# Performance work log

Hardware: AMD Instinct MI355X
Metric: run time of the kernel (lower is better)

Reference implementation:

```python
import jax, jax.numpy as jnp
import numpy as np

RESO = 32          # triplane/voxel resolution
VIT = 16           # ViT patch grid resolution
PAD = 0.1
C_TRI = 64         # triplane channels per plane
C_IMG = 1280       # image feature channels
C_IN = 128         # inner (attention) channels
C_OUT = 64
NH = 8
HD = C_IN // NH
IMG_SIZE = 224.0


def pos_enc(d_model, length):
    pos = jnp.arange(length, dtype=jnp.float32)[:, None]
    div = jnp.exp(jnp.arange(0, d_model, 2, dtype=jnp.float32) * (-np.log(10000.0) / d_model))
    pe = jnp.zeros((length, d_model), jnp.float32)
    pe = pe.at[:, 0::2].set(jnp.sin(pos * div))
    pe = pe.at[:, 1::2].set(jnp.cos(pos * div))
    return pe


def bilinear_sample(feats, gx, gy):
    # feats: [B, J, H, W, C]; gx, gy: [B, J, N] in [-1, 1]; align_corners=True
    B, J, Hh, Ww, _ = feats.shape
    ux = (gx + 1.0) * 0.5 * (Ww - 1)
    uy = (gy + 1.0) * 0.5 * (Hh - 1)
    x0 = jnp.floor(ux).astype(jnp.int32)
    y0 = jnp.floor(uy).astype(jnp.int32)
    wx = (ux - x0)[..., None]
    wy = (uy - y0)[..., None]
    x1 = jnp.clip(x0 + 1, 0, Ww - 1)
    y1 = jnp.clip(y0 + 1, 0, Hh - 1)
    x0 = jnp.clip(x0, 0, Ww - 1)
    y0 = jnp.clip(y0, 0, Hh - 1)
    bi = jnp.arange(B)[:, None, None]
    ji = jnp.arange(J)[None, :, None]
    f00 = feats[bi, ji, y0, x0]
    f01 = feats[bi, ji, y0, x1]
    f10 = feats[bi, ji, y1, x0]
    f11 = feats[bi, ji, y1, x1]
    return (f00 * (1 - wx) * (1 - wy) + f01 * wx * (1 - wy)
            + f10 * (1 - wx) * wy + f11 * wx * wy)


def forward(triplane_feat, image_feat, proj_mat, k_w, k_b, q_w, q_b, v_w, v_b,
            in_w, in_b, out_w, out_b, proj_w, proj_b):
    B, n_img = image_feat.shape[0], image_feat.shape[1]
    N = RESO ** 3
    img = image_feat[:, :, 1:, :]                        # drop CLS -> [B,J,256,C_IMG]
    image_pe = pos_enc(C_IN, VIT * VIT)[None, None]      # [1,1,256,C_IN]
    k_feat = img @ k_w.T + k_b + image_pe
    v_feat = img @ v_w.T + v_b + image_pe
    k_map = k_feat.reshape(B, n_img, VIT, VIT, C_IN)     # [B,J,H,W,C]
    v_map = v_feat.reshape(B, n_img, VIT, VIT, C_IN)

    # voxel coords -> project into each camera
    idx = jnp.arange(RESO)
    X, Y, Z = jnp.meshgrid(idx, idx, idx, indexing='ij')
    vox = jnp.stack([X, Y, Z], -1).reshape(N, 3).astype(jnp.float32)
    vox = (vox / (RESO - 1) - 0.5) * 2.0 * (1.0 + PAD + 1e-5)
    homo = jnp.concatenate([vox, jnp.ones((N, 1), jnp.float32)], -1)  # [N,4]
    pc = jnp.einsum('nk,bjik->bjni', homo, proj_mat)                   # [B,J,N,4]
    px = pc[..., 0] / pc[..., 2]
    py = pc[..., 1] / pc[..., 2]
    gx = jnp.clip((px / (IMG_SIZE - 1) - 0.5) * 2.0, -1.0, 1.0)
    gy = jnp.clip((py / (IMG_SIZE - 1) - 0.5) * 2.0, -1.0, 1.0)
    # The torch code does a 3D grid_sample whose depth coordinate lands exactly
    # on each image index (align_corners=True), so it reduces to per-image
    # bilinear sampling on the 16x16 token maps.
    k_s = bilinear_sample(k_map, gx, gy)   # [B,J,N,C_IN]
    v_s = bilinear_sample(v_map, gx, gy)

    # triplane features expanded to the voxel grid (voxel order n = x*R^2+y*R+z)
    xz, xy, yz = jnp.split(triplane_feat, 3, axis=2)     # each [B,C,R,R]
    xz_t = jnp.transpose(xz, (0, 3, 2, 1))               # [B,x,z,C]
    xy_t = jnp.transpose(xy, (0, 3, 2, 1))               # [B,x,y,C]
    yz_t = jnp.transpose(yz, (0, 3, 2, 1))               # [B,y,z,C]
    shp = (B, RESO, RESO, RESO, C_TRI)
    xz_v = jnp.broadcast_to(xz_t[:, :, None, :, :], shp)
    xy_v = jnp.broadcast_to(xy_t[:, :, :, None, :], shp)
    yz_v = jnp.broadcast_to(yz_t[:, None, :, :, :], shp)
    tri = jnp.concatenate([xz_v, xy_v, yz_v], -1).reshape(B, N, 3 * C_TRI)
    q = tri @ q_w.T + q_b + pos_enc(C_IN, N)[None]       # [B,N,C_IN]

    # per-voxel cross attention (q_len=1, kv_len=n_img); torch MHA semantics
    Wq, Wk, Wv = in_w[:C_IN], in_w[C_IN:2 * C_IN], in_w[2 * C_IN:]
    bq, bk, bv = in_b[:C_IN], in_b[C_IN:2 * C_IN], in_b[2 * C_IN:]
    qh = (q @ Wq.T + bq).reshape(B, N, NH, HD)
    k_t = jnp.transpose(k_s, (0, 2, 1, 3))               # [B,N,J,C]
    v_t = jnp.transpose(v_s, (0, 2, 1, 3))
    kh = (k_t @ Wk.T + bk).reshape(B, N, n_img, NH, HD)
    vh = (v_t @ Wv.T + bv).reshape(B, N, n_img, NH, HD)
    logits = jnp.einsum('bnhd,bnjhd->bnhj', qh, kh) / np.sqrt(HD).astype(np.float32)
    attn = jax.nn.softmax(logits, axis=-1)
    o = jnp.einsum('bnhj,bnjhd->bnhd', attn, vh).reshape(B, N, C_IN)
    o = o @ out_w.T + out_b

    # mean-pool volume back to three planes
    vol = o.reshape(B, RESO, RESO, RESO, C_IN)             # [b,x,y,z,c]
    xz_o = jnp.transpose(vol.mean(axis=2), (0, 2, 1, 3))   # [b,z,x,c]
    xy_o = jnp.transpose(vol.mean(axis=3), (0, 2, 1, 3))   # [b,y,x,c]
    yz_o = jnp.transpose(vol.mean(axis=1), (0, 2, 1, 3))   # [b,z,y,c]
    planes = jnp.concatenate([xz_o, xy_o, yz_o], axis=1)   # [B,3R,R,C_IN]
    out = planes @ proj_w.T + proj_b
    return jnp.transpose(out, (0, 3, 1, 2))                # [B,C_OUT,3R,R]


def setup_inputs() -> dict:
    key = jax.random.key(0)
    ks = jax.random.split(key, 10)
    B, J = 2, 5
    s = 0.02
    base = jnp.array([[200., 0., 112., 0.],
                      [0., 200., 112., 0.],
                      [0., 0., 1., 3.5],
                      [0., 0., 0., 1.]], jnp.float32)
    return {
        'triplane_feat': jax.random.normal(ks[0], (B, C_TRI, 3 * RESO, RESO), jnp.float32),
        'image_feat': jax.random.normal(ks[1], (B, J, VIT * VIT + 1, C_IMG), jnp.float32),
        'proj_mat': base[None, None] + 0.01 * jax.random.normal(ks[2], (B, J, 4, 4), jnp.float32),
        'valid_frames': jnp.ones((B, J), jnp.int32),
        'k_w': s * jax.random.normal(ks[3], (C_IN, C_IMG), jnp.float32), 'k_b': jnp.zeros((C_IN,), jnp.float32),
        'q_w': s * jax.random.normal(ks[4], (C_IN, 3 * C_TRI), jnp.float32), 'q_b': jnp.zeros((C_IN,), jnp.float32),
        'v_w': s * jax.random.normal(ks[5], (C_IN, C_IMG), jnp.float32), 'v_b': jnp.zeros((C_IN,), jnp.float32),
        'in_w': s * jax.random.normal(ks[6], (3 * C_IN, C_IN), jnp.float32), 'in_b': jnp.zeros((3 * C_IN,), jnp.float32),
        'out_w': s * jax.random.normal(ks[7], (C_IN, C_IN), jnp.float32), 'out_b': jnp.zeros((C_IN,), jnp.float32),
        'proj_w': s * jax.random.normal(ks[8], (C_OUT, C_IN), jnp.float32), 'proj_b': jnp.zeros((C_OUT,), jnp.float32),
    }


def reference(triplane_feat, image_feat, proj_mat, valid_frames, k_w, k_b, q_w, q_b,
              v_w, v_b, in_w, in_b, out_w, out_b, proj_w, proj_b):
    # valid_frames matches the torch forward signature but is unused in its body
    return forward(triplane_feat, image_feat, proj_mat, k_w, k_b, q_w, q_b,
                   v_w, v_b, in_w, in_b, out_w, out_b, proj_w, proj_b)
```

## Files before the change

### kernel.cpp

```cpp
#include <hip/hip_runtime.h>
#include <hip/hip_bf16.h>
#include <cstddef>

#define NVOX 32768
#define J5 5
typedef __hip_bfloat16 bf16;
typedef __attribute__((ext_vector_type(8))) short bf16x8v;
typedef __attribute__((ext_vector_type(4))) float f32x4;

static __device__ __forceinline__ float pe_val(int pos, int c) {
  float dv = expf((float)(c & ~1) * (-0.0719557841560639f));
  float arg = (float)pos * dv;
  return (c & 1) ? cosf(arg) : sinf(arg);
}
static __device__ __forceinline__ short f2b(float f) {
  __hip_bfloat16 h = __float2bfloat16(f);
  return *reinterpret_cast<short*>(&h);
}
static __device__ __forceinline__ float b2f(short s) {
  __hip_bfloat16 h = *reinterpret_cast<__hip_bfloat16*>(&s);
  return __bfloat162float(h);
}
static __device__ __forceinline__ float2 cmul(float2 a, float2 b) {
  return make_float2(a.x * b.x - a.y * b.y, a.x * b.y + a.y * b.x);
}

#define NB_TABS   24
#define NB_WQPE   64
#define NB_WQC    96
#define NB_WO     32
#define NB_QCB    1
#define NB_CVT    1600
#define NB_TRI    1536
#define NB_FOLDW  1280
#define NB_PEB    512
#define B_TABS   0
#define B_WQPE   (B_TABS + NB_TABS)
#define B_WQC    (B_WQPE + NB_WQPE)
#define B_WO     (B_WQC + NB_WQC)
#define B_QCB    (B_WO + NB_WO)
#define B_CVT    (B_QCB + NB_QCB)
#define B_TRI    (B_CVT + NB_CVT)
#define B_FOLDW  (B_TRI + NB_TRI)
#define B_PEB    (B_FOLDW + NB_FOLDW)
#define NB_TOTAL (B_PEB + NB_PEB)

__global__ __launch_bounds__(256) void k_prep(
    const float* __restrict__ img, const float* __restrict__ tp,
    const float* __restrict__ k_w, const float* __restrict__ k_b,
    const float* __restrict__ q_w, const float* __restrict__ q_b,
    const float* __restrict__ v_w, const float* __restrict__ v_b,
    const float* __restrict__ in_w, const float* __restrict__ in_b,
    const float* __restrict__ out_w, const float* __restrict__ out_b,
    const float* __restrict__ proj_w, const float* __restrict__ proj_b,
    float2* __restrict__ tabs, short* __restrict__ Wqb_s, float* __restrict__ Wo,
    float* __restrict__ qcb, float* __restrict__ obb, short* __restrict__ imgb,
    short* __restrict__ tri_tb, short* __restrict__ Wkvb_s, float* __restrict__ peb) {
  __shared__ float s_pe[128];
  const int bx = blockIdx.x, t = threadIdx.x;

  if (bx < B_WQPE) {
    int idx = bx * 256 + t;
    if (idx < 6144) {
      int tb = idx >> 11, rem = idx & 2047;
      int pos = rem >> 6, i = rem & 63;
      float dv = expf((float)(2 * i) * (-0.0719557841560639f));
      float mult = (tb == 0) ? 1024.0f : (tb == 1) ? 32.0f : 1.0f;
      float ang = (float)pos * mult * dv;
      tabs[idx] = make_float2(cosf(ang), sinf(ang));
    }
  } else if (bx < B_WQC) {
    int e = (bx - B_WQPE) * 256 + t;
    int c = e >> 7, j = e & 127;
    Wqb_s[(size_t)c * 320 + 192 + j] = f2b(in_w[(size_t)c * 128 + j]);
  } else if (bx < B_WO) {
    int e = (bx - B_WQC) * 256 + t;
    int c = e / 192, k = e % 192;
    const float* ir = in_w + (size_t)c * 128;
    float acc = 0.f;
    for (int j = 0; j < 128; j++) acc = fmaf(ir[j], q_w[(size_t)j * 192 + k], acc);
    Wqb_s[(size_t)c * 320 + k] = f2b(acc);
  } else if (bx < B_QCB) {
    int e = (bx - B_WO) * 256 + t;
    int o = e >> 7, c = e & 127;
    const float* pr = proj_w + (size_t)o * 128;
    float acc = 0.f;
    for (int j = 0; j < 128; j++) acc = fmaf(pr[j], out_w[(size_t)j * 128 + c], acc);
    Wo[e] = acc;
  } else if (bx < B_CVT) {
    if (t < 128) {
      float acc = in_b[t];
      const float* ir = in_w + (size_t)t * 128;
      for (int j = 0; j < 128; j++) acc = fmaf(ir[j], q_b[j], acc);
      qcb[t] = acc;
    }
    if (t < 64) {
      float acc = proj_b[t];
      const float* pr = proj_w + (size_t)t * 128;
      for (int j = 0; j < 128; j++) acc = fmaf(pr[j], out_b[j], acc);
      obb[t] = acc;
    }
  } else if (bx < B_TRI) {
    int e8 = (bx - B_CVT) * 256 + t;
    int row = e8 / 160, k8 = e8 % 160;
    int bj = row >> 8, p = row & 255;
    const float* src = img + ((size_t)(bj * 257 + 1 + p)) * 1280 + k8 * 8;
    float4 a = *(const float4*)src;
    float4 b = *(const float4*)(src + 4);
    bf16x8v v;
    v[0] = f2b(a.x); v[1] = f2b(a.y); v[2] = f2b(a.z); v[3] = f2b(a.w);
    v[4] = f2b(b.x); v[5] = f2b(b.y); v[6] = f2b(b.z); v[7] = f2b(b.w);
    *reinterpret_cast<bf16x8v*>(imgb + (size_t)row * 1280 + k8 * 8) = v;
  } else if (bx < B_FOLDW) {
    int idx = (bx - B_TRI) * 256 + t;
    int cc   = idx & 63;
    int rem  = idx >> 6;
    int cell = rem & 1023;
    int segb = rem >> 10;
    int seg = segb % 3, b = segb / 3;
    int i = cell >> 5, j = cell & 31;
    tri_tb[idx] = f2b(tp[(((size_t)(b * 64 + cc)) * 96 + seg * 32 + i) * 32 + j]);
  } else if (bx < B_PEB) {
    int u = (bx - B_FOLDW) * 256 + t;
    int c = u / 1280, k = u % 1280;
    const float* w = (c < 128) ? k_w : v_w;
    const float* ir = in_w + (size_t)(128 + c) * 128;
    float acc = 0.f;
    for (int j = 0; j < 128; j++) acc = fmaf(ir[j], w[(size_t)j * 1280 + k], acc);
    Wkvb_s[(size_t)c * 1280 + k] = f2b(acc);
  } else {
    int e = bx - B_PEB;
    int which = e >> 8, p = e & 255;
    if (t < 128) {
      const float* bias = which ? v_b : k_b;
      s_pe[t] = bias[t] + pe_val(p, t);
    }
    __syncthreads();
    if (t < 128) {
      int c = t;
      const float* wr = in_w + (size_t)(128 + which * 128 + c) * 128;
      float acc = in_b[128 + which * 128 + c];
      for (int j = 0; j < 128; j++) acc = fmaf(s_pe[j], wr[j], acc);
      peb[((size_t)(which * 256 + p)) * 128 + c] = acc;
    }
  }
}

__global__ __launch_bounds__(256) void k_gemm_kv(
    const short* __restrict__ imgb, const short* __restrict__ Wkvb_s,
    const float* __restrict__ peb, short* __restrict__ k2b, short* __restrict__ v2b) {
  __shared__ __align__(16) short A_lds[64 * 64];
  __shared__ __align__(16) short B_lds[64 * 64];
  const int m0 = blockIdx.x * 64;
  const int nb0 = blockIdx.y * 64;
  const int t = threadIdx.x;
  const int lane = t & 63, w = t >> 6;
  f32x4 acc[4];
#pragma unroll
  for (int f = 0; f < 4; f++) acc[f] = (f32x4){0.f, 0.f, 0.f, 0.f};

  for (int ct = 0; ct < 20; ct++) {
    __syncthreads();
#pragma unroll
    for (int it = 0; it < 2; it++) {
      int u = it * 256 + t;
      int r = u >> 3, g = u & 7;
      {
        const int4 src = *reinterpret_cast<const int4*>(imgb + (size_t)(m0 + r) * 1280 + ct * 64 + g * 8);
        *reinterpret_cast<int4*>(&A_lds[(r * 8 + (g ^ (r & 7))) * 8]) = src;
      }
      {
        const int4 src = *reinterpret_cast<const int4*>(Wkvb_s + (size_t)(nb0 + r) * 1280 + ct * 64 + g * 8);
        *reinterpret_cast<int4*>(&B_lds[(r * 8 + (g ^ (r & 7))) * 8]) = src;
      }
    }
    __syncthreads();
#pragma unroll
    for (int ks = 0; ks < 2; ks++) {
      int arow = w * 16 + (lane & 15);
      int akb = ks * 4 + (lane >> 4);
      bf16x8v a = *reinterpret_cast<const bf16x8v*>(&A_lds[(arow * 8 + (akb ^ (arow & 7))) * 8]);
#pragma unroll
      for (int f = 0; f < 4; f++) {
        int bcol = f * 16 + (lane & 15);
        bf16x8v bb = *reinterpret_cast<const bf16x8v*>(&B_lds[(bcol * 8 + (akb ^ (bcol & 7))) * 8]);
        acc[f] = __builtin_amdgcn_mfma_f32_16x16x32_bf16(a, bb, acc[f], 0, 0, 0);
      }
    }
  }
#pragma unroll
  for (int f = 0; f < 4; f++) {
#pragma unroll
    for (int reg = 0; reg < 4; reg++) {
      int grow = m0 + w * 16 + (lane >> 4) * 4 + reg;
      int gcol = nb0 + f * 16 + (lane & 15);
      int p = grow & 255;
      int which = gcol >> 7, c = gcol & 127;
      float val = acc[f][reg] + peb[((size_t)(which * 256 + p)) * 128 + c];
      short* dst = which ? v2b : k2b;
      dst[(size_t)grow * 128 + c] = f2b(val);
    }
  }
}

__global__ __launch_bounds__(256) void k_main(
    const short* __restrict__ tri_tb, const short* __restrict__ Wqb_s,
    const float* __restrict__ qcb, const float2* __restrict__ tabs,
    const short* __restrict__ k2b, const short* __restrict__ v2b,
    const float* __restrict__ proj, bf16* __restrict__ obuf) {
  __shared__ __align__(16) short A_lds[32 * 64];
  __shared__ __align__(16) short B_lds[128 * 64];
  __shared__ __align__(16) short qh_lds[32 * 128];
  __shared__ __align__(16) ushort sIr[160][4];
  __shared__ __align__(16) float sW4[160][4];
  __shared__ __align__(16) float lg[160 * 8];
  const int b = blockIdx.y;
  const int n0 = blockIdx.x * 32;
  const int t = threadIdx.x;
  const int lane = t & 63, w = t >> 6;
  const int xq = n0 >> 10, yq = (n0 >> 5) & 31;
  const float2* tabX = tabs;
  const float2* tabY = tabs + 2048;
  const float2* tabZ = tabs + 4096;

  if (t < 160) {
    int r = t / J5, j = t % J5;
    int n = n0 + r;
    int x = n >> 10, y = (n >> 5) & 31, z = n & 31;
    const float SC = (float)(1.0 + 0.1 + 1e-05);
    float fx = ((float)x / 31.0f - 0.5f) * 2.0f * SC;
    float fy = ((float)y / 31.0f - 0.5f) * 2.0f * SC;
    float fz = ((float)z / 31.0f - 0.5f) * 2.0f * SC;
    const float* P = proj + (size_t)(b * J5 + j) * 16;
    float pc0 = fmaf(fx, P[0], fmaf(fy, P[1], fmaf(fz, P[2],  P[3])));
    float pc1 = fmaf(fx, P[4], fmaf(fy, P[5], fmaf(fz, P[6],  P[7])));
    float pc2 = fmaf(fx, P[8], fmaf(fy, P[9], fmaf(fz, P[10], P[11])));
    float px = pc0 / pc2, py = pc1 / pc2;
    float gx = fminf(fmaxf((px / 223.0f - 0.5f) * 2.0f, -1.0f), 1.0f);
    float gy = fminf(fmaxf((py / 223.0f - 0.5f) * 2.0f, -1.0f), 1.0f);
    float ux = (gx + 1.0f) * 0.5f * 15.0f;
    float uy = (gy + 1.0f) * 0.5f * 15.0f;
    float fx0 = floorf(ux), fy0 = floorf(uy);
    int x0 = (int)fx0, y0 = (int)fy0;
    float wx = ux - fx0, wy = uy - fy0;
    int x1 = min(x0 + 1, 15), y1 = min(y0 + 1, 15);
    x0 = min(max(x0, 0), 15); y0 = min(max(y0, 0), 15);
    int rowb = (b * J5 + j) * 256;
    sIr[t][0] = (ushort)(rowb + y0 * 16 + x0);
    sIr[t][1] = (ushort)(rowb + y0 * 16 + x1);
    sIr[t][2] = (ushort)(rowb + y1 * 16 + x0);
    sIr[t][3] = (ushort)(rowb + y1 * 16 + x1);
    sW4[t][0] = (1.f - wx) * (1.f - wy);
    sW4[t][1] = wx * (1.f - wy);
    sW4[t][2] = (1.f - wx) * wy;
    sW4[t][3] = wx * wy;
  }

  f32x4 acc[2][2];
#pragma unroll
  for (int m = 0; m < 2; m++)
#pragma unroll
    for (int f = 0; f < 2; f++) acc[m][f] = (f32x4){0.f, 0.f, 0.f, 0.f};

  for (int ct = 0; ct < 5; ct++) {
    __syncthreads();
    {
      int r = t >> 3, g = t & 7;
      if (ct < 3) {
        int n = n0 + r;
        int x = n >> 10, y = (n >> 5) & 31, z = n & 31;
        int cell = (ct == 0) ? (z * 32 + x) : (ct == 1) ? (y * 32 + x) : (z * 32 + y);
        const int4 src = *reinterpret_cast<const int4*>(
            tri_tb + ((size_t)(b * 3 + ct) * 1024 + cell) * 64 + g * 8);
        *reinterpret_cast<int4*>(&A_lds[(r * 8 + (g ^ (r & 7))) * 8]) = src;
      } else {
        int i0 = (ct - 3) * 32 + g * 4;
        bf16x8v v;
#pragma unroll
        for (int q = 0; q < 4; q++) {
          int i = i0 + q;
          float2 exy = cmul(tabX[xq * 64 + i], tabY[yq * 64 + i]);
          float2 e = cmul(exy, tabZ[r * 64 + i]);
          v[q * 2]     = f2b(e.y);
          v[q * 2 + 1] = f2b(e.x);
        }
        *reinterpret_cast<bf16x8v*>(&A_lds[(r * 8 + (g ^ (r & 7))) * 8]) = v;
      }
    }
    {
#pragma unroll
      for (int it = 0; it < 4; it++) {
        int u = it * 256 + t;
        int col = u >> 3, g = u & 7;
        const int4 src = *reinterpret_cast<const int4*>(
            Wqb_s + (size_t)col * 320 + ct * 64 + g * 8);
        *reinterpret_cast<int4*>(&B_lds[(col * 8 + (g ^ (col & 7))) * 8]) = src;
      }
    }
    __syncthreads();
#pragma unroll
    for (int ks = 0; ks < 2; ks++) {
      int kb = ks * 4 + (lane >> 4);
      bf16x8v a[2], bb[2];
#pragma unroll
      for (int m = 0; m < 2; m++) {
        int row = m * 16 + (lane & 15);
        a[m] = *reinterpret_cast<const bf16x8v*>(&A_lds[(row * 8 + (kb ^ (row & 7))) * 8]);
      }
#pragma unroll
      for (int f = 0; f < 2; f++) {
        int col = w * 32 + f * 16 + (lane & 15);
        bb[f] = *reinterpret_cast<const bf16x8v*>(&B_lds[(col * 8 + (kb ^ (col & 7))) * 8]);
      }
#pragma unroll
      for (int m = 0; m < 2; m++)
#pragma unroll
        for (int f = 0; f < 2; f++)
          acc[m][f] = __builtin_amdgcn_mfma_f32_16x16x32_bf16(a[m], bb[f], acc[m][f], 0, 0, 0);
    }
  }
#pragma unroll
  for (int m = 0; m < 2; m++)
#pragma unroll
    for (int f = 0; f < 2; f++)
#pragma unroll
      for (int reg = 0; reg < 4; reg++) {
        int row = m * 16 + (lane >> 4) * 4 + reg;
        int col = w * 32 + f * 16 + (lane & 15);
        qh_lds[row * 128 + col] = f2b(acc[m][f][reg] + qcb[col]);
      }
  __syncthreads();

  {
    const int oct = t & 15, rjIdx = t >> 4;
    const int c0 = oct * 8;
#pragma unroll
    for (int it = 0; it < 10; it++) {
      int rj = rjIdx + it * 16;
      int r = rj / J5;
      ushort4 I4 = *reinterpret_cast<const ushort4*>(sIr[rj]);
      float4 W4 = *reinterpret_cast<const float4*>(sW4[rj]);
      bf16x8v t0 = *reinterpret_cast<const bf16x8v*>(k2b + (size_t)I4.x * 128 + c0);
      bf16x8v t1 = *reinterpret_cast<const bf16x8v*>(k2b + (size_t)I4.y * 128 + c0);
      bf16x8v t2 = *reinterpret_cast<const bf16x8v*>(k2b + (size_t)I4.z * 128 + c0);
      bf16x8v t3 = *reinterpret_cast<const bf16x8v*>(k2b + (size_t)I4.w * 128 + c0);
      bf16x8v q8 = *reinterpret_cast<const bf16x8v*>(&qh_lds[r * 128 + c0]);
      float pv = 0.f;
#pragma unroll
      for (int e = 0; e < 8; e++) {
        float kh = fmaf(W4.x, b2f(t0[e]), fmaf(W4.y, b2f(t1[e]),
                   fmaf(W4.z, b2f(t2[e]), W4.w * b2f(t3[e]))));
        pv = fmaf(b2f(q8[e]), kh, pv);
      }
      pv += __shfl_xor(pv, 1);
      if (!(oct & 1)) lg[rj * 8 + (oct >> 1)] = pv * 0.25f;
    }
  }
  __syncthreads();

  {
    int r = t >> 3, h = t & 7;
    float l[J5];
    float m = -1e30f;
#pragma unroll
    for (int j = 0; j < J5; j++) { l[j] = lg[(r * J5 + j) * 8 + h]; m = fmaxf(m, l[j]); }
    float sden = 0.f;
#pragma unroll
    for (int j = 0; j < J5; j++) { l[j] = expf(l[j] - m); sden += l[j]; }
    float inv = 1.0f / sden;
#pragma unroll
    for (int j = 0; j < J5; j++) lg[(r * J5 + j) * 8 + h] = l[j] * inv;
  }
  __syncthreads();

  {
    const int oct = t & 15;
    const int c0 = oct * 8;
#pragma unroll
    for (int it = 0; it < 2; it++) {
      int r = (t >> 4) + it * 16;
      float o8[8] = {0.f, 0.f, 0.f, 0.f, 0.f, 0.f, 0.f, 0.f};
#pragma unroll
      for (int j = 0; j < J5; j++) {
        int rj = r * J5 + j;
        float aw = lg[rj * 8 + (oct >> 1)];
        ushort4 I4 = *reinterpret_cast<const ushort4*>(sIr[rj]);
        float4 W4 = *reinterpret_cast<const float4*>(sW4[rj]);
        float w0 = aw * W4.x, w1 = aw * W4.y, w2 = aw * W4.z, w3 = aw * W4.w;
        bf16x8v t0 = *reinterpret_cast<const bf16x8v*>(v2b + (size_t)I4.x * 128 + c0);
        bf16x8v t1 = *reinterpret_cast<const bf16x8v*>(v2b + (size_t)I4.y * 128 + c0);
        bf16x8v t2 = *reinterpret_cast<const bf16x8v*>(v2b + (size_t)I4.z * 128 + c0);
        bf16x8v t3 = *reinterpret_cast<const bf16x8v*>(v2b + (size_t)I4.w * 128 + c0);
#pragma unroll
        for (int e = 0; e < 8; e++) {
          o8[e] = fmaf(w0, b2f(t0[e]), o8[e]);
          o8[e] = fmaf(w1, b2f(t1[e]), o8[e]);
          o8[e] = fmaf(w2, b2f(t2[e]), o8[e]);
          o8[e] = fmaf(w3, b2f(t3[e]), o8[e]);
        }
      }
      bf16x8v out;
#pragma unroll
      for (int e = 0; e < 8; e++) out[e] = f2b(o8[e]);
      *reinterpret_cast<bf16x8v*>((short*)obuf + ((size_t)b * NVOX + n0 + r) * 128 + c0) = out;
    }
  }
}

__global__ __launch_bounds__(128) void k_reduce(const bf16* __restrict__ obuf,
                                                float* __restrict__ pacc) {
  int blk = blockIdx.x;
  int b = blockIdx.y;
  int t = threadIdx.x;
  int quad = t & 31, sub = t >> 5;
  int c0 = quad * 4;
  int cell = blk * 4 + sub;
  const ushort* ob = (const ushort*)obuf + (size_t)b * NVOX * 128;
  float4 acc = {0.f, 0.f, 0.f, 0.f};
  if (cell < 1024) {
    int z = cell >> 5, x = cell & 31;
    for (int y = 0; y < 32; y++) {
      ushort4 u = *(const ushort4*)(ob + ((size_t)(x * 1024 + y * 32 + z) * 128 + c0));
      acc.x += b2f((short)u.x); acc.y += b2f((short)u.y);
      acc.z += b2f((short)u.z); acc.w += b2f((short)u.w);
    }
    *(float4*)(&pacc[((size_t)(b * 96 + z) * 32 + x) * 128 + c0]) = acc;
  } else if (cell < 2048) {
    int e = cell - 1024;
    int y = e >> 5, x = e & 31;
    for (int z = 0; z < 32; z++) {
      ushort4 u = *(const ushort4*)(ob + ((size_t)(x * 1024 + y * 32 + z) * 128 + c0));
      acc.x += b2f((short)u.x); acc.y += b2f((short)u.y);
      acc.z += b2f((short)u.z); acc.w += b2f((short)u.w);
    }
    *(float4*)(&pacc[((size_t)(b * 96 + 32 + y) * 32 + x) * 128 + c0]) = acc;
  } else {
    int e = cell - 2048;
    int z = e >> 5, y = e & 31;
    for (int x = 0; x < 32; x++) {
      ushort4 u = *(const ushort4*)(ob + ((size_t)(x * 1024 + y * 32 + z) * 128 + c0));
      acc.x += b2f((short)u.x); acc.y += b2f((short)u.y);
      acc.z += b2f((short)u.z); acc.w += b2f((short)u.w);
    }
    *(float4*)(&pacc[((size_t)(b * 96 + 64 + z) * 32 + y) * 128 + c0]) = acc;
  }
}

__global__ __launch_bounds__(128) void k_final(
    const float* __restrict__ pacc, const float* __restrict__ Wo,
    const float* __restrict__ obb, float* __restrict__ outp) {
  int bp = blockIdx.x;
  int b = bp / 96, prow = bp % 96;
  int obase = blockIdx.y * 16;
  __shared__ __align__(16) float lds[32 * 129];
  for (int idx = threadIdx.x; idx < 4096; idx += 128) {
    int col = idx >> 7, k = idx & 127;
    lds[col * 129 + k] = pacc[(size_t)bp * 32 * 128 + idx] * (1.0f / 32.0f);
  }
  __syncthreads();
  for (int e = threadIdx.x; e < 16 * 32; e += 128) {
    int o = obase + (e >> 5), col = e & 31;
    float val = obb[o];
    const float* wr = Wo + (size_t)o * 128;
    const float* lr = lds + col * 129;
    for (int k = 0; k < 128; k++) val = fmaf(wr[k], lr[k], val);
    outp[((size_t)(b * 64 + o) * 96 + prow) * 32 + col] = val;
  }
}

extern "C" void kernel_launch(void* const* d_in, const int* in_sizes, int n_in,
                              void* d_out, int out_size, void* d_ws, size_t ws_size,
                              hipStream_t stream) {
  const float* tp     = (const float*)d_in[0];
  const float* img    = (const float*)d_in[1];
  const float* proj   = (const float*)d_in[2];
  const float* k_w    = (const float*)d_in[4];
  const float* k_b    = (const float*)d_in[5];
  const float* q_w    = (const float*)d_in[6];
  const float* q_b    = (const float*)d_in[7];
  const float* v_w    = (const float*)d_in[8];
  const float* v_b    = (const float*)d_in[9];
  const float* in_w   = (const float*)d_in[10];
  const float* in_b   = (const float*)d_in[11];
  const float* out_w  = (const float*)d_in[12];
  const float* out_b  = (const float*)d_in[13];
  const float* proj_w = (const float*)d_in[14];
  const float* proj_b = (const float*)d_in[15];
  const int B = 2;

  float* ws = (float*)d_ws;
  size_t off = 0;
  short*  tri_tb = (short*)(ws + off);  off += 196608;
  short*  Wkvb_s = (short*)(ws + off);  off += 163840;
  short*  Wqb_s  = (short*)(ws + off);  off += 20480;
  float*  peb    = ws + off;            off += 65536;
  float2* tabs   = (float2*)(ws + off); off += 12288;
  float*  qcb    = ws + off;            off += 128;
  float*  Wo     = ws + off;            off += 8192;
  float*  obb    = ws + off;            off += 64;
  short*  k2b    = (short*)(ws + off);  off += 163840;
  short*  v2b    = (short*)(ws + off);  off += 163840;
  float*  pacc   = ws + off;            off += 786432;
  float*  zone   = ws + off;            off += 4194304;
  short*  imgb   = (short*)zone;
  bf16*   obuf   = (bf16*)zone;
  if (ws_size < off * sizeof(float)) return;

  k_prep<<<dim3(NB_TOTAL), dim3(256), 0, stream>>>(
      img, tp, k_w, k_b, q_w, q_b, v_w, v_b, in_w, in_b, out_w, out_b, proj_w, proj_b,
      tabs, Wqb_s, Wo, qcb, obb, imgb, tri_tb, Wkvb_s, peb);
  k_gemm_kv<<<dim3(40, 4), dim3(256), 0, stream>>>(imgb, Wkvb_s, peb, k2b, v2b);
  k_main<<<dim3(NVOX / 32, B), dim3(256), 0, stream>>>(
      tri_tb, Wqb_s, qcb, tabs, k2b, v2b, proj, obuf);
  k_reduce<<<dim3(768, B), dim3(128), 0, stream>>>(obuf, pacc);
  k_final<<<dim3(B * 96, 4), dim3(128), 0, stream>>>(pacc, Wo, obb, (float*)d_out);
}
```

Before: 117.5 us.

## Fold PE and bias into KV GEMM K-dim, retile GEMM, drop Wq LDS staging, widen reduce

```diff
diff --git a/kernel.cpp b/kernel.cpp
--- a/kernel.cpp
+++ b/kernel.cpp
@@ -4,6 +4,7 @@
 
 #define NVOX 32768
 #define J5 5
+#define KB2 1472
 typedef __hip_bfloat16 bf16;
 typedef __attribute__((ext_vector_type(8))) short bf16x8v;
 typedef __attribute__((ext_vector_type(4))) float f32x4;
@@ -33,7 +34,9 @@
 #define NB_CVT    1600
 #define NB_TRI    1536
 #define NB_FOLDW  1280
-#define NB_PEB    512
+#define NB_PETAB  128
+#define NB_WIN    128
+#define NB_CB     1
 #define B_TABS   0
 #define B_WQPE   (B_TABS + NB_TABS)
 #define B_WQC    (B_WQPE + NB_WQPE)
@@ -42,8 +45,10 @@
 #define B_CVT    (B_QCB + NB_QCB)
 #define B_TRI    (B_CVT + NB_CVT)
 #define B_FOLDW  (B_TRI + NB_TRI)
-#define B_PEB    (B_FOLDW + NB_FOLDW)
-#define NB_TOTAL (B_PEB + NB_PEB)
+#define B_PETAB  (B_FOLDW + NB_FOLDW)
+#define B_WIN    (B_PETAB + NB_PETAB)
+#define B_CB     (B_WIN + NB_WIN)
+#define NB_TOTAL (B_CB + NB_CB)
 
 __global__ __launch_bounds__(256) void k_prep(
     const float* __restrict__ img, const float* __restrict__ tp,
@@ -55,8 +60,7 @@
     const float* __restrict__ proj_w, const float* __restrict__ proj_b,
     float2* __restrict__ tabs, short* __restrict__ Wqb_s, float* __restrict__ Wo,
     float* __restrict__ qcb, float* __restrict__ obb, short* __restrict__ imgb,
-    short* __restrict__ tri_tb, short* __restrict__ Wkvb_s, float* __restrict__ peb) {
-  __shared__ float s_pe[128];
+    short* __restrict__ tri_tb, short* __restrict__ Wkvb2, short* __restrict__ pe_tab) {
   const int bx = blockIdx.x, t = threadIdx.x;
 
   if (bx < B_WQPE) {
@@ -120,85 +124,98 @@
     int seg = segb % 3, b = segb / 3;
     int i = cell >> 5, j = cell & 31;
     tri_tb[idx] = f2b(tp[(((size_t)(b * 64 + cc)) * 96 + seg * 32 + i) * 32 + j]);
-  } else if (bx < B_PEB) {
+  } else if (bx < B_PETAB) {
     int u = (bx - B_FOLDW) * 256 + t;
     int c = u / 1280, k = u % 1280;
     const float* w = (c < 128) ? k_w : v_w;
     const float* ir = in_w + (size_t)(128 + c) * 128;
     float acc = 0.f;
     for (int j = 0; j < 128; j++) acc = fmaf(ir[j], w[(size_t)j * 1280 + k], acc);
-    Wkvb_s[(size_t)c * 1280 + k] = f2b(acc);
+    Wkvb2[(size_t)c * KB2 + k] = f2b(acc);
+  } else if (bx < B_WIN) {
+    int e = (bx - B_PETAB) * 256 + t;
+    int p = e >> 7, c = e & 127;
+    pe_tab[e] = f2b(pe_val(p, c));
+  } else if (bx < B_CB) {
+    int e = (bx - B_WIN) * 256 + t;
+    int c = e >> 7, j = e & 127;
+    Wkvb2[(size_t)c * KB2 + 1280 + j] = f2b(in_w[(size_t)(128 + c) * 128 + j]);
   } else {
-    int e = bx - B_PEB;
-    int which = e >> 8, p = e & 255;
-    if (t < 128) {
-      const float* bias = which ? v_b : k_b;
-      s_pe[t] = bias[t] + pe_val(p, t);
-    }
-    __syncthreads();
-    if (t < 128) {
-      int c = t;
-      const float* wr = in_w + (size_t)(128 + which * 128 + c) * 128;
-      float acc = in_b[128 + which * 128 + c];
-      for (int j = 0; j < 128; j++) acc = fmaf(s_pe[j], wr[j], acc);
-      peb[((size_t)(which * 256 + p)) * 128 + c] = acc;
-    }
+    int c = t;
+    int which = c >> 7;
+    const float* bias = which ? v_b : k_b;
+    const float* ir = in_w + (size_t)(128 + c) * 128;
+    float acc = in_b[128 + c];
+    for (int j = 0; j < 128; j++) acc = fmaf(bias[j], ir[j], acc);
+    short* row = Wkvb2 + (size_t)c * KB2 + 1408;
+    row[0] = f2b(acc);
+    for (int k = 1; k < 64; k++) row[k] = 0;
   }
 }
 
 __global__ __launch_bounds__(256) void k_gemm_kv(
-    const short* __restrict__ imgb, const short* __restrict__ Wkvb_s,
-    const float* __restrict__ peb, short* __restrict__ k2b, short* __restrict__ v2b) {
-  __shared__ __align__(16) short A_lds[64 * 64];
+    const short* __restrict__ imgb, const short* __restrict__ Wkvb2,
+    const short* __restrict__ pe_tab, short* __restrict__ k2b, short* __restrict__ v2b) {
+  __shared__ __align__(16) short A_lds[32 * 64];
   __shared__ __align__(16) short B_lds[64 * 64];
-  const int m0 = blockIdx.x * 64;
+  const int m0 = blockIdx.x * 32;
   const int nb0 = blockIdx.y * 64;
   const int t = threadIdx.x;
   const int lane = t & 63, w = t >> 6;
-  f32x4 acc[4];
-#pragma unroll
-  for (int f = 0; f < 4; f++) acc[f] = (f32x4){0.f, 0.f, 0.f, 0.f};
-
-  for (int ct = 0; ct < 20; ct++) {
+  const int wm = w & 1, wn = w >> 1;
+  f32x4 acc[2];
+  acc[0] = (f32x4){0.f, 0.f, 0.f, 0.f};
+  acc[1] = (f32x4){0.f, 0.f, 0.f, 0.f};
+
+  for (int ct = 0; ct < 23; ct++) {
     __syncthreads();
-#pragma unroll
-    for (int it = 0; it < 2; it++) {
-      int u = it * 256 + t;
-      int r = u >> 3, g = u & 7;
-      {
-        const int4 src = *reinterpret_cast<const int4*>(imgb + (size_t)(m0 + r) * 1280 + ct * 64 + g * 8);
-        *reinterpret_cast<int4*>(&A_lds[(r * 8 + (g ^ (r & 7))) * 8]) = src;
-      }
-      {
-        const int4 src = *reinterpret_cast<const int4*>(Wkvb_s + (size_t)(nb0 + r) * 1280 + ct * 64 + g * 8);
-        *reinterpret_cast<int4*>(&B_lds[(r * 8 + (g ^ (r & 7))) * 8]) = src;
+    {
+      int r = t >> 3, g = t & 7;
+      bf16x8v v;
+      if (ct < 20) {
+        v = *reinterpret_cast<const bf16x8v*>(imgb + (size_t)(m0 + r) * 1280 + ct * 64 + g * 8);
+      } else if (ct < 22) {
+        int p = (m0 + r) & 255;
+        v = *reinterpret_cast<const bf16x8v*>(pe_tab + (size_t)p * 128 + (ct - 20) * 64 + g * 8);
+      } else {
+        v = (bf16x8v){0, 0, 0, 0, 0, 0, 0, 0};
+        if (g == 0) v[0] = (short)0x3F80;
+      }
+      *reinterpret_cast<bf16x8v*>(&A_lds[(r * 8 + (g ^ (r & 7))) * 8]) = v;
+    }
+    {
+#pragma unroll
+      for (int it = 0; it < 2; it++) {
+        int u = it * 256 + t;
+        int r2 = u >> 3, g = u & 7;
+        const int4 src = *reinterpret_cast<const int4*>(
+            Wkvb2 + (size_t)(nb0 + r2) * KB2 + ct * 64 + g * 8);
+        *reinterpret_cast<int4*>(&B_lds[(r2 * 8 + (g ^ (r2 & 7))) * 8]) = src;
       }
     }
     __syncthreads();
 #pragma unroll
     for (int ks = 0; ks < 2; ks++) {
-      int arow = w * 16 + (lane & 15);
-      int akb = ks * 4 + (lane >> 4);
-      bf16x8v a = *reinterpret_cast<const bf16x8v*>(&A_lds[(arow * 8 + (akb ^ (arow & 7))) * 8]);
-#pragma unroll
-      for (int f = 0; f < 4; f++) {
-        int bcol = f * 16 + (lane & 15);
-        bf16x8v bb = *reinterpret_cast<const bf16x8v*>(&B_lds[(bcol * 8 + (akb ^ (bcol & 7))) * 8]);
+      int kb = ks * 4 + (lane >> 4);
+      int arow = wm * 16 + (lane & 15);
+      bf16x8v a = *reinterpret_cast<const bf16x8v*>(&A_lds[(arow * 8 + (kb ^ (arow & 7))) * 8]);
+#pragma unroll
+      for (int f = 0; f < 2; f++) {
+        int bcol = wn * 32 + f * 16 + (lane & 15);
+        bf16x8v bb = *reinterpret_cast<const bf16x8v*>(&B_lds[(bcol * 8 + (kb ^ (bcol & 7))) * 8]);
         acc[f] = __builtin_amdgcn_mfma_f32_16x16x32_bf16(a, bb, acc[f], 0, 0, 0);
       }
     }
   }
 #pragma unroll
-  for (int f = 0; f < 4; f++) {
+  for (int f = 0; f < 2; f++) {
 #pragma unroll
     for (int reg = 0; reg < 4; reg++) {
-      int grow = m0 + w * 16 + (lane >> 4) * 4 + reg;
-      int gcol = nb0 + f * 16 + (lane & 15);
-      int p = grow & 255;
+      int grow = m0 + wm * 16 + (lane >> 4) * 4 + reg;
+      int gcol = nb0 + wn * 32 + f * 16 + (lane & 15);
       int which = gcol >> 7, c = gcol & 127;
-      float val = acc[f][reg] + peb[((size_t)(which * 256 + p)) * 128 + c];
       short* dst = which ? v2b : k2b;
-      dst[(size_t)grow * 128 + c] = f2b(val);
+      dst[(size_t)grow * 128 + c] = f2b(acc[f][reg]);
     }
   }
 }
@@ -209,7 +226,6 @@
     const short* __restrict__ k2b, const short* __restrict__ v2b,
     const float* __restrict__ proj, bf16* __restrict__ obuf) {
   __shared__ __align__(16) short A_lds[32 * 64];
-  __shared__ __align__(16) short B_lds[128 * 64];
   __shared__ __align__(16) short qh_lds[32 * 128];
   __shared__ __align__(16) ushort sIr[160][4];
   __shared__ __align__(16) float sW4[160][4];
@@ -287,30 +303,20 @@
         *reinterpret_cast<bf16x8v*>(&A_lds[(r * 8 + (g ^ (r & 7))) * 8]) = v;
       }
     }
-    {
-#pragma unroll
-      for (int it = 0; it < 4; it++) {
-        int u = it * 256 + t;
-        int col = u >> 3, g = u & 7;
-        const int4 src = *reinterpret_cast<const int4*>(
-            Wqb_s + (size_t)col * 320 + ct * 64 + g * 8);
-        *reinterpret_cast<int4*>(&B_lds[(col * 8 + (g ^ (col & 7))) * 8]) = src;
-      }
-    }
     __syncthreads();
 #pragma unroll
     for (int ks = 0; ks < 2; ks++) {
       int kb = ks * 4 + (lane >> 4);
       bf16x8v a[2], bb[2];
 #pragma unroll
+      for (int f = 0; f < 2; f++) {
+        int col = w * 32 + f * 16 + (lane & 15);
+        bb[f] = *reinterpret_cast<const bf16x8v*>(Wqb_s + (size_t)col * 320 + ct * 64 + kb * 8);
+      }
+#pragma unroll
       for (int m = 0; m < 2; m++) {
         int row = m * 16 + (lane & 15);
         a[m] = *reinterpret_cast<const bf16x8v*>(&A_lds[(row * 8 + (kb ^ (row & 7))) * 8]);
-      }
-#pragma unroll
-      for (int f = 0; f < 2; f++) {
-        int col = w * 32 + f * 16 + (lane & 15);
-        bb[f] = *reinterpret_cast<const bf16x8v*>(&B_lds[(col * 8 + (kb ^ (col & 7))) * 8]);
       }
 #pragma unroll
       for (int m = 0; m < 2; m++)
@@ -412,38 +418,41 @@
   int blk = blockIdx.x;
   int b = blockIdx.y;
   int t = threadIdx.x;
-  int quad = t & 31, sub = t >> 5;
-  int c0 = quad * 4;
-  int cell = blk * 4 + sub;
-  const ushort* ob = (const ushort*)obuf + (size_t)b * NVOX * 128;
-  float4 acc = {0.f, 0.f, 0.f, 0.f};
+  int oct = t & 15, sub = t >> 4;
+  int c0 = oct * 8;
+  int cell = blk * 8 + sub;
+  const short* ob = (const short*)obuf + (size_t)b * NVOX * 128;
+  float a8[8] = {0.f, 0.f, 0.f, 0.f, 0.f, 0.f, 0.f, 0.f};
+  size_t prow;
   if (cell < 1024) {
     int z = cell >> 5, x = cell & 31;
     for (int y = 0; y < 32; y++) {
-      ushort4 u = *(const ushort4*)(ob + ((size_t)(x * 1024 + y * 32 + z) * 128 + c0));
-      acc.x += b2f((short)u.x); acc.y += b2f((short)u.y);
-      acc.z += b2f((short)u.z); acc.w += b2f((short)u.w);
-    }
-    *(float4*)(&pacc[((size_t)(b * 96 + z) * 32 + x) * 128 + c0]) = acc;
+      bf16x8v u = *reinterpret_cast<const bf16x8v*>(ob + ((size_t)(x * 1024 + y * 32 + z) * 128 + c0));
+#pragma unroll
+      for (int e = 0; e < 8; e++) a8[e] += b2f(u[e]);
+    }
+    prow = ((size_t)(b * 96 + z) * 32 + x) * 128 + c0;
   } else if (cell < 2048) {
-    int e = cell - 1024;
-    int y = e >> 5, x = e & 31;
+    int e2 = cell - 1024;
+    int y = e2 >> 5, x = e2 & 31;
     for (int z = 0; z < 32; z++) {
-      ushort4 u = *(const ushort4*)(ob + ((size_t)(x * 1024 + y * 32 + z) * 128 + c0));
-      acc.x += b2f((short)u.x); acc.y += b2f((short)u.y);
-      acc.z += b2f((short)u.z); acc.w += b2f((short)u.w);
-    }
-    *(float4*)(&pacc[((size_t)(b * 96 + 32 + y) * 32 + x) * 128 + c0]) = acc;
+      bf16x8v u = *reinterpret_cast<const bf16x8v*>(ob + ((size_t)(x * 1024 + y * 32 + z) * 128 + c0));
+#pragma unroll
+      for (int e = 0; e < 8; e++) a8[e] += b2f(u[e]);
+    }
+    prow = ((size_t)(b * 96 + 32 + y) * 32 + x) * 128 + c0;
   } else {
-    int e = cell - 2048;
-    int z = e >> 5, y = e & 31;
+    int e2 = cell - 2048;
+    int z = e2 >> 5, y = e2 & 31;
     for (int x = 0; x < 32; x++) {
-      ushort4 u = *(const ushort4*)(ob + ((size_t)(x * 1024 + y * 32 + z) * 128 + c0));
-      acc.x += b2f((short)u.x); acc.y += b2f((short)u.y);
-      acc.z += b2f((short)u.z); acc.w += b2f((short)u.w);
-    }
-    *(float4*)(&pacc[((size_t)(b * 96 + 64 + z) * 32 + y) * 128 + c0]) = acc;
-  }
+      bf16x8v u = *reinterpret_cast<const bf16x8v*>(ob + ((size_t)(x * 1024 + y * 32 + z) * 128 + c0));
+#pragma unroll
+      for (int e = 0; e < 8; e++) a8[e] += b2f(u[e]);
+    }
+    prow = ((size_t)(b * 96 + 64 + z) * 32 + y) * 128 + c0;
+  }
+  *(float4*)(&pacc[prow])     = (float4){a8[0], a8[1], a8[2], a8[3]};
+  *(float4*)(&pacc[prow + 4]) = (float4){a8[4], a8[5], a8[6], a8[7]};
 }
 
 __global__ __launch_bounds__(128) void k_final(
@@ -491,9 +500,9 @@
   float* ws = (float*)d_ws;
   size_t off = 0;
   short*  tri_tb = (short*)(ws + off);  off += 196608;
-  short*  Wkvb_s = (short*)(ws + off);  off += 163840;
+  short*  Wkvb2  = (short*)(ws + off);  off += 188416;
   short*  Wqb_s  = (short*)(ws + off);  off += 20480;
-  float*  peb    = ws + off;            off += 65536;
+  short*  pe_tab = (short*)(ws + off);  off += 16384;
   float2* tabs   = (float2*)(ws + off); off += 12288;
   float*  qcb    = ws + off;            off += 128;
   float*  Wo     = ws + off;            off += 8192;
@@ -508,10 +517,10 @@
 
   k_prep<<<dim3(NB_TOTAL), dim3(256), 0, stream>>>(
       img, tp, k_w, k_b, q_w, q_b, v_w, v_b, in_w, in_b, out_w, out_b, proj_w, proj_b,
-      tabs, Wqb_s, Wo, qcb, obb, imgb, tri_tb, Wkvb_s, peb);
-  k_gemm_kv<<<dim3(40, 4), dim3(256), 0, stream>>>(imgb, Wkvb_s, peb, k2b, v2b);
+      tabs, Wqb_s, Wo, qcb, obb, imgb, tri_tb, Wkvb2, pe_tab);
+  k_gemm_kv<<<dim3(80, 4), dim3(256), 0, stream>>>(imgb, Wkvb2, pe_tab, k2b, v2b);
   k_main<<<dim3(NVOX / 32, B), dim3(256), 0, stream>>>(
       tri_tb, Wqb_s, qcb, tabs, k2b, v2b, proj, obuf);
-  k_reduce<<<dim3(768, B), dim3(128), 0, stream>>>(obuf, pacc);
+  k_reduce<<<dim3(384, B), dim3(128), 0, stream>>>(obuf, pacc);
   k_final<<<dim3(B * 96, 4), dim3(128), 0, stream>>>(pacc, Wo, obb, (float*)d_out);
 }
```

New measurement: 120.3 us. 1.02x slower.
